# Performance work log

Hardware: AMD Instinct MI355X
Metric: run time of the kernel (lower is better)

## Reference

```python
import jax, jax.numpy as jnp
import numpy as np

B, T, FEAT = 16, 800, 120
H, L, C, NL = 512, 4, 5000, 100
KW, PAD = 100, 50


def _lstm_dir(xs, mask, Wih, Whh, b, reverse):
    # xs: [T,B,in], mask: [T,B,1] bool. PyTorch packed-seq semantics:
    # outputs are zero at padded steps, hidden state is held (not updated).
    def step(carry, inp):
        h, c = carry
        xt, mt = inp
        gates = xt @ Wih.T + h @ Whh.T + b  # [B,4H]
        i, f, g, o = jnp.split(gates, 4, axis=1)
        i = jax.nn.sigmoid(i); f = jax.nn.sigmoid(f)
        g = jnp.tanh(g); o = jax.nn.sigmoid(o)
        cn = f * c + i * g
        hn = o * jnp.tanh(cn)
        h2 = jnp.where(mt, hn, h)
        c2 = jnp.where(mt, cn, c)
        return (h2, c2), jnp.where(mt, hn, 0.0)
    Bn = xs.shape[1]
    init = (jnp.zeros((Bn, H), xs.dtype), jnp.zeros((Bn, H), xs.dtype))
    _, ys = jax.lax.scan(step, init, (xs, mask), reverse=reverse)
    return ys  # [T,B,H]


def _forward(x, target, lengths, Wih0, Whh0, b0, WihL, WhhL, bL,
             W_se, W_he, b_he, W_ee, conv_w, W_fe, W_sy, W_gy, b_gy,
             W_yy, b_yy, W_ys, W_ss, W_gs, b_gs):
    Bn, Tn = x.shape[0], x.shape[1]
    xs = x.transpose(1, 0, 2)  # [T,B,F]
    mask = (jnp.arange(Tn)[:, None] < lengths[None, :])[:, :, None]  # [T,B,1]
    h = xs
    for l in range(L):  # 4-layer bidirectional encoder (eval mode: no dropout)
        if l == 0:
            Wf, Wb, Uf, Ub, bf, bb = Wih0[0], Wih0[1], Whh0[0], Whh0[1], b0[0], b0[1]
        else:
            Wf, Wb = WihL[l-1, 0], WihL[l-1, 1]
            Uf, Ub = WhhL[l-1, 0], WhhL[l-1, 1]
            bf, bb = bL[l-1, 0], bL[l-1, 1]
        yf = _lstm_dir(h, mask, Wf, Uf, bf, False)
        yb = _lstm_dir(h, mask, Wb, Ub, bb, True)
        h = jnp.concatenate([yf, yb], axis=2)  # [T,B,2H]
    hbatch = h.transpose(1, 0, 2)  # [B,T,2H]
    e_mask = mask[:, :, 0].T.astype(hbatch.dtype)  # [B,T]
    he_pre = hbatch @ W_he.T + b_he  # precompute L_he(hbatch) once (constant over steps)

    def dec_step(carry, tgt_t):
        s, c, alpha = carry  # s,c: [B,H], alpha: [B,T]
        conv = jax.lax.conv_general_dilated(
            alpha[:, None, :], conv_w, (1,), [(PAD, PAD)],
            dimension_numbers=('NCH', 'OIH', 'NCH'))[:, :, :Tn]  # [B,10,T]
        loc = jnp.einsum('bft,df->btd', conv, W_fe)  # [B,T,2H]
        e = jnp.einsum('btd,d->bt',
                       jnp.tanh((s @ W_se.T)[:, None, :] + he_pre + loc), W_ee[0])
        en = jnp.exp(e - e.max(axis=1, keepdims=True)) * e_mask
        a = en / en.sum(axis=1, keepdims=True)  # [B,T]
        g = jnp.einsum('bt,btd->bd', a, hbatch)  # [B,2H]
        y = jnp.tanh(g @ W_gy.T + b_gy + s @ W_sy.T) @ W_yy.T + b_yy  # [B,C]
        rec = tgt_t @ W_ys.T + s @ W_ss.T + g @ W_gs.T + b_gs  # [B,4H]
        i, f, cg, o = jnp.split(rec, 4, axis=1)
        i = jnp.tanh(i * 0.5) * 0.5 + 0.5
        f = jnp.tanh(f * 0.5) * 0.5 + 0.5
        cg = jnp.tanh(cg)
        o = jnp.tanh(o * 0.5) * 0.5 + 0.5
        cn = f * c + i * cg
        sn = o * jnp.tanh(cn)
        return (sn, cn, a), y

    init = (jnp.zeros((Bn, H), x.dtype), jnp.zeros((Bn, H), x.dtype),
            jnp.zeros((Bn, Tn), x.dtype))
    _, ys = jax.lax.scan(dec_step, init, target.transpose(1, 0, 2))
    return ys.transpose(1, 0, 2)  # [B,NL,C]


def setup_inputs() -> dict:
    key = jax.random.key(0)
    it = iter(jax.random.split(key, 32))
    def rn(shape, scale=0.05):
        return (jax.random.normal(next(it), shape) * scale).astype(jnp.float32)
    inp = {}
    inp['x'] = rn((B, T, FEAT), 1.0)
    inp['lengths'] = jnp.sort(jax.random.randint(next(it), (B,), 600, T + 1, dtype=jnp.int32))[::-1]
    inp['target'] = rn((B, NL, C), 1.0)
    inp['Wih0'] = rn((2, 4 * H, FEAT)); inp['Whh0'] = rn((2, 4 * H, H)); inp['b0'] = rn((2, 4 * H))
    inp['WihL'] = rn((L - 1, 2, 4 * H, 2 * H)); inp['WhhL'] = rn((L - 1, 2, 4 * H, H)); inp['bL'] = rn((L - 1, 2, 4 * H))
    inp['W_se'] = rn((2 * H, H)); inp['W_he'] = rn((2 * H, 2 * H)); inp['b_he'] = rn((2 * H,))
    inp['W_ee'] = rn((1, 2 * H)); inp['conv_w'] = rn((10, 1, KW)); inp['W_fe'] = rn((2 * H, 10))
    inp['W_sy'] = rn((H, H)); inp['W_gy'] = rn((H, 2 * H)); inp['b_gy'] = rn((H,))
    inp['W_yy'] = rn((C, H)); inp['b_yy'] = rn((C,)); inp['W_ys'] = rn((4 * H, C))
    inp['W_ss'] = rn((4 * H, H)); inp['W_gs'] = rn((4 * H, 2 * H)); inp['b_gs'] = rn((4 * H,))
    return inp


def reference(x, lengths, target, Wih0, Whh0, b0, WihL, WhhL, bL,
              W_se, W_he, b_he, W_ee, conv_w, W_fe, W_sy, W_gy, b_gy,
              W_yy, b_yy, W_ys, W_ss, W_gs, b_gs):
    return _forward(x, target, lengths, Wih0, Whh0, b0, WihL, WhhL, bL,
                    W_se, W_he, b_he, W_ee, conv_w, W_fe, W_sy, W_gy, b_gy,
                    W_yy, b_yy, W_ys, W_ss, W_gs, b_gs)
```

## Files before the change

kernel.cpp:

```cpp
#include <hip/hip_runtime.h>
#include <math.h>


#define T_    800
#define B_    16
#define FEAT_ 120
#define H_    512
#define H2_   1024
#define H4_   2048
#define CC_   5000
#define NL_   100
#define CH_   25
#define NCH_  32
#define HPAD  536

typedef __attribute__((ext_vector_type(8))) short bf16x8;
typedef __attribute__((ext_vector_type(4))) float f32x4;

__device__ __forceinline__ void coh_store_f32(float* p, float v) {
  asm volatile("global_store_dword %0, %1, off sc0 sc1"
               :: "v"(p), "v"(v) : "memory");
}
__device__ __forceinline__ void coh_load8_f4(
    const float* p0, const float* p1, const float* p2, const float* p3,
    const float* p4, const float* p5, const float* p6, const float* p7,
    f32x4* o)
{
  asm volatile(
      "global_load_dwordx4 %0, %8, off sc0 sc1\n\t"
      "global_load_dwordx4 %1, %9, off sc0 sc1\n\t"
      "global_load_dwordx4 %2, %10, off sc0 sc1\n\t"
      "global_load_dwordx4 %3, %11, off sc0 sc1\n\t"
      "global_load_dwordx4 %4, %12, off sc0 sc1\n\t"
      "global_load_dwordx4 %5, %13, off sc0 sc1\n\t"
      "global_load_dwordx4 %6, %14, off sc0 sc1\n\t"
      "global_load_dwordx4 %7, %15, off sc0 sc1\n\t"
      "s_waitcnt vmcnt(0)"
      : "=&v"(o[0]), "=&v"(o[1]), "=&v"(o[2]), "=&v"(o[3]),
        "=&v"(o[4]), "=&v"(o[5]), "=&v"(o[6]), "=&v"(o[7])
      : "v"(p0), "v"(p1), "v"(p2), "v"(p3), "v"(p4), "v"(p5), "v"(p6), "v"(p7)
      : "memory");
}

__device__ __forceinline__ unsigned short f2bf(float f) {
  unsigned u = __builtin_bit_cast(unsigned, f);
  u += 0x7FFFu + ((u >> 16) & 1u);
  return (unsigned short)(u >> 16);
}
__device__ __forceinline__ float bf2f(unsigned short s) {
  return __builtin_bit_cast(float, (unsigned)s << 16);
}

#define GBM 128
#define GBN 128
#define GBK 32
#define LDT 40

__device__ void mfma_gemm_tile(
    const float* __restrict__ A, const float* __restrict__ W,
    const float* __restrict__ bias, float* __restrict__ C,
    int M, int N, int K, int ldc, int bx, int by,
    unsigned short* As, unsigned short* Ws)
{
  const int tid = threadIdx.x;
  const int row0 = by * GBM, col0 = bx * GBN;
  const int lane = tid & 63, w = tid >> 6;
  const int wr = w >> 1, wc = w & 1;
  const int lm = lane & 15, lk8 = (lane >> 4) * 8;

  f32x4 acc[4][4];
#pragma unroll
  for (int i = 0; i < 4; i++)
#pragma unroll
    for (int j = 0; j < 4; j++) acc[i][j] = (f32x4)(0.f);

  const int sr = tid >> 1, skh = (tid & 1) * 16;

  for (int kt = 0; kt < K; kt += GBK) {
    {
      const int ar = row0 + sr;
      const int wrow = col0 + sr;
      unsigned short abuf[16], wbuf[16];
#pragma unroll
      for (int q = 0; q < 4; q++) {
        const int k0 = kt + skh + q * 4;
        float4 av = make_float4(0.f, 0.f, 0.f, 0.f);
        float4 wv = make_float4(0.f, 0.f, 0.f, 0.f);
        if (k0 + 4 <= K) {
          if (ar < M)   av = *(const float4*)(A + (size_t)ar * K + k0);
          if (wrow < N) wv = *(const float4*)(W + (size_t)wrow * K + k0);
        }
        abuf[q*4+0] = f2bf(av.x); abuf[q*4+1] = f2bf(av.y);
        abuf[q*4+2] = f2bf(av.z); abuf[q*4+3] = f2bf(av.w);
        wbuf[q*4+0] = f2bf(wv.x); wbuf[q*4+1] = f2bf(wv.y);
        wbuf[q*4+2] = f2bf(wv.z); wbuf[q*4+3] = f2bf(wv.w);
      }
      __syncthreads();
      *(uint4*)(As + sr * LDT + skh)     = *(uint4*)(abuf);
      *(uint4*)(As + sr * LDT + skh + 8) = *(uint4*)(abuf + 8);
      *(uint4*)(Ws + sr * LDT + skh)     = *(uint4*)(wbuf);
      *(uint4*)(Ws + sr * LDT + skh + 8) = *(uint4*)(wbuf + 8);
      __syncthreads();
    }
    bf16x8 af[4], bfv[4];
#pragma unroll
    for (int mi = 0; mi < 4; mi++)
      af[mi] = *(const bf16x8*)(As + (wr * 64 + mi * 16 + lm) * LDT + lk8);
#pragma unroll
    for (int ni = 0; ni < 4; ni++)
      bfv[ni] = *(const bf16x8*)(Ws + (wc * 64 + ni * 16 + lm) * LDT + lk8);
#pragma unroll
    for (int mi = 0; mi < 4; mi++)
#pragma unroll
      for (int ni = 0; ni < 4; ni++)
        acc[mi][ni] = __builtin_amdgcn_mfma_f32_16x16x32_bf16(
            af[mi], bfv[ni], acc[mi][ni], 0, 0, 0);
  }
#pragma unroll
  for (int mi = 0; mi < 4; mi++) {
#pragma unroll
    for (int reg = 0; reg < 4; reg++) {
      const int row = row0 + wr * 64 + mi * 16 + (lane >> 4) * 4 + reg;
      if (row < M) {
        float* crow = C + (size_t)row * ldc;
#pragma unroll
        for (int ni = 0; ni < 4; ni++) {
          const int col = col0 + wc * 64 + ni * 16 + lm;
          crow[col] = acc[mi][ni][reg] + (bias ? bias[col] : 0.f);
        }
      }
    }
  }
}

__global__ __launch_bounds__(256) void gemm_mfma(
    const float* __restrict__ A, const float* __restrict__ W,
    const float* __restrict__ bias, float* __restrict__ C,
    int M, int N, int K, int ldc)
{
  __shared__ unsigned short As[GBM * LDT];
  __shared__ unsigned short Ws[GBN * LDT];
  mfma_gemm_tile(A, W, bias, C, M, N, K, ldc, blockIdx.x, blockIdx.y, As, Ws);
}

__global__ __launch_bounds__(256) void gemm_mfma_dual(
    const float* __restrict__ A0, const float* __restrict__ W0,
    const float* __restrict__ b0, float* __restrict__ C0,
    const float* __restrict__ A1, const float* __restrict__ W1,
    const float* __restrict__ b1, float* __restrict__ C1,
    int M, int N, int K, int ldc)
{
  __shared__ unsigned short As[GBM * LDT];
  __shared__ unsigned short Ws[GBN * LDT];
  if (blockIdx.z == 0)
    mfma_gemm_tile(A0, W0, b0, C0, M, N, K, ldc, blockIdx.x, blockIdx.y, As, Ws);
  else
    mfma_gemm_tile(A1, W1, b1, C1, M, N, K, ldc, blockIdx.x, blockIdx.y, As, Ws);
}

__global__ __launch_bounds__(256) void transpose_x(
    const float* __restrict__ x, float* __restrict__ xt)
{
  const int i = blockIdx.x * 256 + threadIdx.x;
  if (i >= T_ * B_ * FEAT_) return;
  const int f = i % FEAT_;
  const int r = i / FEAT_;
  const int b = r % B_;
  const int t = r / B_;
  xt[i] = x[((long)b * T_ + t) * FEAT_ + f];
}

__global__ __launch_bounds__(256, 1) void lstm_fused(
    const float* __restrict__ gxF, const float* __restrict__ gxB,
    float* __restrict__ gxFn, float* __restrict__ gxBn,
    const float* __restrict__ inbF, const float* __restrict__ inbB,
    const float* __restrict__ WihF_, const float* __restrict__ WihB_,
    const float* __restrict__ bF_, const float* __restrict__ bB_, int Kin,
    float* __restrict__ hg0, float* __restrict__ hg1,
    float* __restrict__ cg, float* __restrict__ outb,
    const float* __restrict__ WhhF, const float* __restrict__ WhhB,
    const int* __restrict__ lengths, int s0, int pbase,
    unsigned* __restrict__ bar)
{
  __shared__ unsigned short h_hi[16][HPAD];
  __shared__ unsigned short h_lo[16][HPAD];
  __shared__ float gl[128 * 16];
  __shared__ float c_l[512];
  __shared__ int   len_l[16];
  __shared__ unsigned short As[GBM * LDT];
  __shared__ unsigned short Ws[GBN * LDT];

  if (blockIdx.x >= 32) {
    if (inbF == nullptr) return;
    const int g = blockIdx.x - 32;
    const int bx = g & 15, by = (g >> 4) & 3, bz = g >> 6;
    if (bz == 0)
      mfma_gemm_tile(inbF, WihF_, bF_, gxFn, CH_ * B_, H4_, Kin, H4_, bx, by, As, Ws);
    else
      mfma_gemm_tile(inbB, WihB_, bB_, gxBn, CH_ * B_, H4_, Kin, H4_, bx, by, As, Ws);
    return;
  }

  const int wg  = blockIdx.x;
  const int dir = wg >> 4;
  const int m   = wg & 15;
  const int tid = threadIdx.x;
  const int lane = tid & 63, w = tid >> 6;
  const int lrow = lane & 15, lko = (lane >> 4) * 8;

  if (tid < 16) len_l[tid] = lengths[tid];
  {
    const int eA = tid, eB = tid + 256;
    c_l[eA] = cg[(dir * 16 + (eA & 15)) * 512 + m * 32 + (eA >> 4)];
    c_l[eB] = cg[(dir * 16 + (eB & 15)) * 512 + m * 32 + (eB >> 4)];
  }

  const float* Whh = dir ? WhhB : WhhF;
  bf16x8 whi[2][16], wlo[2][16];
#pragma unroll
  for (int rt = 0; rt < 2; rt++) {
    const int row128 = (w * 2 + rt) * 16 + lrow;
    const int g = row128 >> 5, jj = row128 & 31;
    const float* wr = Whh + (size_t)(g * 512 + m * 32 + jj) * 512 + lko;
#pragma unroll
    for (int kt = 0; kt < 16; kt++) {
      unsigned short h8[8], l8[8];
#pragma unroll
      for (int i = 0; i < 8; i++) {
        const float v = wr[kt * 32 + i];
        h8[i] = f2bf(v);
        l8[i] = f2bf(v - bf2f(h8[i]));
      }
      whi[rt][kt] = *(bf16x8*)h8;
      wlo[rt][kt] = *(bf16x8*)l8;
    }
  }
  __syncthreads();

  unsigned* bcnt = bar + dir * 32;

  const int b0  = tid & 15;
  const int jjA = tid >> 4;
  const int jjB = jjA + 16;
  const int gb_ = tid >> 4;
  const int gk0 = (tid & 15) * 32;

  for (int ls = 0; ls < CH_; ls++) {
    const int s = s0 + ls;
    const int lt = dir ? (CH_ - 1 - ls) : ls;
    const float* gxp = (dir ? gxB : gxF) + ((size_t)lt * 16 + b0) * 2048 + m * 32;
    float ga[4], gb[4];
#pragma unroll
    for (int g = 0; g < 4; g++) { ga[g] = gxp[g * 512 + jjA]; gb[g] = gxp[g * 512 + jjB]; }

    if (s == 0) {
      const uint4 z = make_uint4(0, 0, 0, 0);
#pragma unroll
      for (int o = 0; o < 4; o++) {
        *(uint4*)&h_hi[gb_][gk0 + o * 8] = z;
        *(uint4*)&h_lo[gb_][gk0 + o * 8] = z;
      }
    } else {
      const float* hsrc = ((s & 1) ? hg1 : hg0) + (dir * 16 + gb_) * 512 + gk0;
      f32x4 hv[8];
      coh_load8_f4(hsrc, hsrc + 4, hsrc + 8, hsrc + 12,
                   hsrc + 16, hsrc + 20, hsrc + 24, hsrc + 28, hv);
      unsigned short sh[32], sl[32];
#pragma unroll
      for (int q = 0; q < 8; q++)
#pragma unroll
        for (int i = 0; i < 4; i++) {
          const float v = hv[q][i];
          const unsigned short hh = f2bf(v);
          sh[q * 4 + i] = hh;
          sl[q * 4 + i] = f2bf(v - bf2f(hh));
        }
#pragma unroll
      for (int o = 0; o < 4; o++) {
        *(uint4*)&h_hi[gb_][gk0 + o * 8] = *(uint4*)(sh + o * 8);
        *(uint4*)&h_lo[gb_][gk0 + o * 8] = *(uint4*)(sl + o * 8);
      }
    }
    __syncthreads();

    f32x4 acc[2];
    acc[0] = (f32x4)(0.f); acc[1] = (f32x4)(0.f);
#pragma unroll
    for (int kt = 0; kt < 16; kt++) {
      const bf16x8 bh = *(const bf16x8*)&h_hi[lrow][kt * 32 + lko];
      const bf16x8 bl = *(const bf16x8*)&h_lo[lrow][kt * 32 + lko];
#pragma unroll
      for (int rt = 0; rt < 2; rt++) {
        acc[rt] = __builtin_amdgcn_mfma_f32_16x16x32_bf16(whi[rt][kt], bh, acc[rt], 0, 0, 0);
        acc[rt] = __builtin_amdgcn_mfma_f32_16x16x32_bf16(wlo[rt][kt], bh, acc[rt], 0, 0, 0);
        acc[rt] = __builtin_amdgcn_mfma_f32_16x16x32_bf16(whi[rt][kt], bl, acc[rt], 0, 0, 0);
      }
    }
#pragma unroll
    for (int rt = 0; rt < 2; rt++) {
      const int rbase = (w * 2 + rt) * 16 + (lane >> 4) * 4;
#pragma unroll
      for (int r = 0; r < 4; r++)
        gl[(rbase + r) * 16 + lrow] = acc[rt][r];
    }
    __syncthreads();

    const int t = dir ? (T_ - 1 - s) : s;
    const bool mk = t < len_l[b0];
    float houtA, houtB, hnA, hnB;
    {
      const float gi = gl[(0 * 32 + jjA) * 16 + b0] + ga[0];
      const float gf = gl[(1 * 32 + jjA) * 16 + b0] + ga[1];
      const float gc = gl[(2 * 32 + jjA) * 16 + b0] + ga[2];
      const float go = gl[(3 * 32 + jjA) * 16 + b0] + ga[3];
      const float iv = 1.f / (1.f + expf(-gi));
      const float fv = 1.f / (1.f + expf(-gf));
      const float gv = tanhf(gc);
      const float ov = 1.f / (1.f + expf(-go));
      const float c_old = c_l[tid];
      const float h_old = bf2f(h_hi[b0][m * 32 + jjA]) + bf2f(h_lo[b0][m * 32 + jjA]);
      const float cn = fv * c_old + iv * gv;
      hnA = ov * tanhf(cn);
      c_l[tid] = mk ? cn : c_old;
      houtA = mk ? hnA : h_old;
    }
    {
      const float gi = gl[(0 * 32 + jjB) * 16 + b0] + gb[0];
      const float gf = gl[(1 * 32 + jjB) * 16 + b0] + gb[1];
      const float gc = gl[(2 * 32 + jjB) * 16 + b0] + gb[2];
      const float go = gl[(3 * 32 + jjB) * 16 + b0] + gb[3];
      const float iv = 1.f / (1.f + expf(-gi));
      const float fv = 1.f / (1.f + expf(-gf));
      const float gv = tanhf(gc);
      const float ov = 1.f / (1.f + expf(-go));
      const float c_old = c_l[tid + 256];
      const float h_old = bf2f(h_hi[b0][m * 32 + jjB]) + bf2f(h_lo[b0][m * 32 + jjB]);
      const float cn = fv * c_old + iv * gv;
      hnB = ov * tanhf(cn);
      c_l[tid + 256] = mk ? cn : c_old;
      houtB = mk ? hnB : h_old;
    }
    {
      float* hdst = ((s & 1) ? hg0 : hg1) + (dir * 16 + b0) * 512 + m * 32;
      coh_store_f32(&hdst[jjA], houtA);
      coh_store_f32(&hdst[jjB], houtB);
    }
    asm volatile("s_waitcnt vmcnt(0)" ::: "memory");
    __syncthreads();
    if (ls != CH_ - 1 && tid == 0) {
      __hip_atomic_fetch_add(bcnt, 1u, __ATOMIC_RELAXED, __HIP_MEMORY_SCOPE_AGENT);
      const unsigned tgt = (unsigned)(pbase + ls + 1) * 16u;
      long tries = 0;
      while (__hip_atomic_load(bcnt, __ATOMIC_RELAXED,
                               __HIP_MEMORY_SCOPE_AGENT) < tgt) {
        if (++tries > (1L << 22)) break;
      }
    }
    __syncthreads();
    outb[((size_t)t * 16 + b0) * H2_ + dir * 512 + m * 32 + jjA] = mk ? hnA : 0.f;
    outb[((size_t)t * 16 + b0) * H2_ + dir * 512 + m * 32 + jjB] = mk ? hnB : 0.f;
  }
  {
    const int eA = tid, eB = tid + 256;
    cg[(dir * 16 + (eA & 15)) * 512 + m * 32 + (eA >> 4)] = c_l[eA];
    cg[(dir * 16 + (eB & 15)) * 512 + m * 32 + (eB >> 4)] = c_l[eB];
  }
}

__device__ __forceinline__ float dot512(const float* s, const float* w) {
  float acc = 0.f;
#pragma unroll 4
  for (int k = 0; k < 512; k += 4) {
    float4 sv = *(const float4*)(s + k);
    float4 wv = *(const float4*)(w + k);
    acc = fmaf(sv.x, wv.x, acc); acc = fmaf(sv.y, wv.y, acc);
    acc = fmaf(sv.z, wv.z, acc); acc = fmaf(sv.w, wv.w, acc);
  }
  return acc;
}
__device__ __forceinline__ float dot1024(const float* s, const float* w) {
  float acc = 0.f;
#pragma unroll 4
  for (int k = 0; k < 1024; k += 4) {
    float4 sv = *(const float4*)(s + k);
    float4 wv = *(const float4*)(w + k);
    acc = fmaf(sv.x, wv.x, acc); acc = fmaf(sv.y, wv.y, acc);
    acc = fmaf(sv.z, wv.z, acc); acc = fmaf(sv.w, wv.w, acc);
  }
  return acc;
}

__global__ __launch_bounds__(256) void dec_f1(
    const float* __restrict__ alpha, const float* __restrict__ cw,
    float* __restrict__ conv,
    const float* __restrict__ sdec, const float* __restrict__ W_se,
    float* __restrict__ sebuf)
{
  const int wg = blockIdx.x, tid = threadIdx.x;
  if (wg < 500) {
    const int idx = wg * 256 + tid;
    if (idx >= B_ * 10 * T_) return;
    const int t = idx % T_;
    const int f = (idx / T_) % 10;
    const int b = idx / (10 * T_);
    const float* a = alpha + b * T_;
    const float* w = cw + f * 100;
    float acc = 0.f;
    const int k0 = (50 - t) > 0 ? (50 - t) : 0;
    const int k1 = (T_ + 50 - t) < 100 ? (T_ + 50 - t) : 100;
    for (int k = k0; k < k1; k++) acc = fmaf(a[t + k - 50], w[k], acc);
    conv[idx] = acc;
  } else {
    const int idx = (wg - 500) * 256 + tid;
    const int b = idx & 15, n = idx >> 4;
    sebuf[(size_t)b * H2_ + n] = dot512(sdec + (size_t)b * H_, W_se + (size_t)n * H_);
  }
}

__global__ __launch_bounds__(256) void att_e(
    const float* __restrict__ se, const float* __restrict__ he,
    const float* __restrict__ conv, const float* __restrict__ W_fe,
    const float* __restrict__ W_ee, float* __restrict__ e)
{
  __shared__ float wfe[10240];
  __shared__ float ses[1024];
  __shared__ float wee[1024];
  __shared__ float red[4];
  const int wg = blockIdx.x;
  const int b = wg / 50, t0 = (wg % 50) * 16;
  const int tid = threadIdx.x;
  for (int i = tid; i < 10240; i += 256) wfe[i] = W_fe[i];
  for (int i = tid; i < 1024; i += 256) {
    ses[i] = se[b * H2_ + i];
    wee[i] = W_ee[i];
  }
  __syncthreads();
  for (int tt = 0; tt < 16; tt++) {
    const int t = t0 + tt;
    float cv[10];
#pragma unroll
    for (int f = 0; f < 10; f++) cv[f] = conv[(b * 10 + f) * T_ + t];
    const float* hrow = he + ((long)t * B_ + b) * H2_;
    float part = 0.f;
#pragma unroll
    for (int q = 0; q < 4; q++) {
      const int d = tid + q * 256;
      float loc = 0.f;
      const float* wf = &wfe[d * 10];
#pragma unroll
      for (int f = 0; f < 10; f++) loc = fmaf(cv[f], wf[f], loc);
      const float val = tanhf(ses[d] + hrow[d] + loc);
      part = fmaf(val, wee[d], part);
    }
#pragma unroll
    for (int off = 32; off; off >>= 1) part += __shfl_down(part, off);
    if ((tid & 63) == 0) red[tid >> 6] = part;
    __syncthreads();
    if (tid == 0) e[b * T_ + t] = red[0] + red[1] + red[2] + red[3];
    __syncthreads();
  }
}

__global__ __launch_bounds__(256) void att_sg(
    const float* __restrict__ e, const int* __restrict__ lengths,
    const float* __restrict__ hb, float* __restrict__ alpha,
    float* __restrict__ g)
{
  __shared__ float al[800];
  __shared__ float red[4];
  __shared__ float bc, bc2;
  const int wg = blockIdx.x;
  const int b = wg >> 2, dg = wg & 3;
  const int tid = threadIdx.x;
  const int len = lengths[b];
  float v[4];
  float mx = -1e30f;
#pragma unroll
  for (int q = 0; q < 4; q++) {
    const int t = tid + q * 256;
    v[q] = (t < T_) ? e[b * T_ + t] : -1e30f;
    mx = fmaxf(mx, v[q]);
  }
#pragma unroll
  for (int off = 32; off; off >>= 1) mx = fmaxf(mx, __shfl_down(mx, off));
  if ((tid & 63) == 0) red[tid >> 6] = mx;
  __syncthreads();
  if (tid == 0) bc = fmaxf(fmaxf(red[0], red[1]), fmaxf(red[2], red[3]));
  __syncthreads();
  const float m = bc;
  float ex[4];
  float s = 0.f;
#pragma unroll
  for (int q = 0; q < 4; q++) {
    const int t = tid + q * 256;
    ex[q] = (t < T_ && t < len) ? expf(v[q] - m) : 0.f;
    s += ex[q];
  }
#pragma unroll
  for (int off = 32; off; off >>= 1) s += __shfl_down(s, off);
  __syncthreads();
  if ((tid & 63) == 0) red[tid >> 6] = s;
  __syncthreads();
  if (tid == 0) bc2 = red[0] + red[1] + red[2] + red[3];
  __syncthreads();
  const float inv = 1.f / bc2;
#pragma unroll
  for (int q = 0; q < 4; q++) {
    const int t = tid + q * 256;
    if (t < T_) al[t] = ex[q] * inv;
  }
  __syncthreads();
  if (dg == 0) {
#pragma unroll
    for (int q = 0; q < 4; q++) {
      const int t = tid + q * 256;
      if (t < T_) alpha[b * T_ + t] = al[t];
    }
  }
  const int d = dg * 256 + tid;
  const float* hp = hb + (size_t)b * H2_ + d;
  float acc = 0.f;
#pragma unroll 8
  for (int t = 0; t < T_; t++)
    acc = fmaf(al[t], hp[(size_t)t * B_ * H2_], acc);
  g[b * H2_ + d] = acc;
}

__global__ __launch_bounds__(256) void dec_f4(
    const float* __restrict__ gvec, const float* __restrict__ sdec,
    const float* __restrict__ W_gy, const float* __restrict__ W_sy,
    const float* __restrict__ b_gy, float* __restrict__ zvec,
    const float* __restrict__ W_ss, const float* __restrict__ W_gs,
    const float* __restrict__ pre, float* __restrict__ rec)
{
  const int wg = blockIdx.x, tid = threadIdx.x;
  if (wg < 32) {
    const int idx = wg * 256 + tid;
    const int b = idx & 15, n = idx >> 4;
    float acc = b_gy[n];
    acc += dot1024(gvec + (size_t)b * H2_, W_gy + (size_t)n * H2_);
    acc += dot512(sdec + (size_t)b * H_, W_sy + (size_t)n * H_);
    zvec[(size_t)b * H_ + n] = tanhf(acc);
  } else {
    const int idx = (wg - 32) * 256 + tid;
    const int b = idx & 15, n = idx >> 4;
    float acc = pre[(size_t)b * NL_ * H4_ + n];
    acc += dot512(sdec + (size_t)b * H_, W_ss + (size_t)n * H_);
    acc += dot1024(gvec + (size_t)b * H2_, W_gs + (size_t)n * H2_);
    rec[(size_t)b * H4_ + n] = acc;
  }
}

__global__ __launch_bounds__(256) void dec_f5(
    const float* __restrict__ zvec, const float* __restrict__ W_yy,
    const float* __restrict__ b_yy, float* __restrict__ outp,
    const float* __restrict__ rec, float* __restrict__ s,
    float* __restrict__ c)
{
  const int wg = blockIdx.x, tid = threadIdx.x;
  if (wg < 313) {
    const int idx = wg * 256 + tid;
    if (idx >= B_ * CC_) return;
    const int b = idx & 15, n = idx >> 4;
    float acc = b_yy[n];
    acc += dot512(zvec + (size_t)b * H_, W_yy + (size_t)n * H_);
    outp[(size_t)b * NL_ * CC_ + n] = acc;
  } else {
    const int idx = (wg - 313) * 256 + tid;
    const int jj = idx & 511, b = idx >> 9;
    const float* r = rec + b * H4_;
    const float gi = r[jj], gf = r[jj + 512], gc = r[jj + 1024], go = r[jj + 1536];
    const float iv = tanhf(gi * 0.5f) * 0.5f + 0.5f;
    const float fv = tanhf(gf * 0.5f) * 0.5f + 0.5f;
    const float cgv = tanhf(gc);
    const float ov = tanhf(go * 0.5f) * 0.5f + 0.5f;
    const float cn = fv * c[idx] + iv * cgv;
    const float sn = ov * tanhf(cn);
    c[idx] = cn;
    s[idx] = sn;
  }
}

extern "C" void kernel_launch(void* const* d_in, const int* in_sizes, int n_in,
                              void* d_out, int out_size, void* d_ws, size_t ws_size,
                              hipStream_t stream)
{
  const float* x       = (const float*)d_in[0];
  const int*   lengths = (const int*)  d_in[1];
  const float* target  = (const float*)d_in[2];
  const float* Wih0    = (const float*)d_in[3];
  const float* Whh0    = (const float*)d_in[4];
  const float* b0      = (const float*)d_in[5];
  const float* WihL    = (const float*)d_in[6];
  const float* WhhL    = (const float*)d_in[7];
  const float* bL      = (const float*)d_in[8];
  const float* W_se    = (const float*)d_in[9];
  const float* W_he    = (const float*)d_in[10];
  const float* b_he    = (const float*)d_in[11];
  const float* W_ee    = (const float*)d_in[12];
  const float* conv_w  = (const float*)d_in[13];
  const float* W_fe    = (const float*)d_in[14];
  const float* W_sy    = (const float*)d_in[15];
  const float* W_gy    = (const float*)d_in[16];
  const float* b_gy    = (const float*)d_in[17];
  const float* W_yy    = (const float*)d_in[18];
  const float* b_yy    = (const float*)d_in[19];
  const float* W_ys    = (const float*)d_in[20];
  const float* W_ss    = (const float*)d_in[21];
  const float* W_gs    = (const float*)d_in[22];
  const float* b_gs    = (const float*)d_in[23];
  float* out = (float*)d_out;

  const size_t CHB4 = (size_t)CH_ * B_ * H4_;
  float* bufA = (float*)d_ws;
  float* bufB = bufA + (size_t)T_ * B_ * H2_;
  float* gxc0 = bufB + (size_t)T_ * B_ * H2_;
  float* gxc1 = gxc0 + 2 * CHB4;
  float* he   = bufB;
  float* ysp  = gxc0;
  float* st   = gxc1 + 2 * CHB4;
  float* hg0  = st;
  float* hg1  = hg0 + 2 * B_ * H_;
  float* cg   = hg1 + 2 * B_ * H_;
  float* sdec = cg + 2 * B_ * H_;
  float* cdec = sdec + B_ * H_;
  float* alpha= cdec + B_ * H_;
  float* conv = alpha + B_ * T_;
  float* ebuf = conv + B_ * 10 * T_;
  float* sebuf= ebuf + B_ * T_;
  float* gvec = sebuf + B_ * H2_;
  float* zvec = gvec + B_ * H2_;
  float* rec  = zvec + B_ * H_;
  unsigned* bar = (unsigned*)(rec + B_ * H4_ + 32);

  (void)hipMemsetAsync(bar, 0, 2048, stream);

  transpose_x<<<(T_ * B_ * FEAT_ + 255) / 256, 256, 0, stream>>>(x, bufA);

  float* inb  = bufA;
  float* outb = bufB;
  float* gx[2] = {gxc0, gxc1};
  for (int l = 0; l < 4; l++) {
    const int Kin = (l == 0) ? FEAT_ : H2_;
    const float *WihF, *WihB, *WhhF, *WhhB, *bF, *bB;
    if (l == 0) {
      WihF = Wih0;                 WihB = Wih0 + (size_t)H4_ * FEAT_;
      WhhF = Whh0;                 WhhB = Whh0 + (size_t)H4_ * H_;
      bF = b0;                     bB = b0 + H4_;
    } else {
      const size_t o = (size_t)(l - 1) * 2;
      WihF = WihL + o * H4_ * H2_; WihB = WihF + (size_t)H4_ * H2_;
      WhhF = WhhL + o * H4_ * H_;  WhhB = WhhF + (size_t)H4_ * H_;
      bF = bL + o * H4_;           bB = bF + H4_;
    }
    (void)hipMemsetAsync(hg0, 0, (size_t)3 * 2 * B_ * H_ * sizeof(float), stream);
    {
      dim3 gg(H4_ / GBN, (CH_ * B_ + GBM - 1) / GBM, 2);
      gemm_mfma_dual<<<gg, 256, 0, stream>>>(
          inb, WihF, bF, gx[0],
          inb + (size_t)(T_ - CH_) * B_ * Kin, WihB, bB, gx[0] + CHB4,
          CH_ * B_, H4_, Kin, H4_);
    }
    for (int c = 0; c < NCH_; c++) {
      const int cur = c & 1, nxt = cur ^ 1;
      const bool hasNext = (c + 1 < NCH_);
      const float* inbFn = hasNext ? inb + (size_t)(c + 1) * CH_ * B_ * Kin : nullptr;
      const float* inbBn = hasNext ? inb + (size_t)(T_ - (c + 2) * CH_) * B_ * Kin : nullptr;
      lstm_fused<<<160, 256, 0, stream>>>(
          gx[cur], gx[cur] + CHB4, gx[nxt], gx[nxt] + CHB4,
          inbFn, inbBn, WihF, WihB, bF, bB, Kin,
          hg0, hg1, cg, outb, WhhF, WhhB, lengths,
          c * CH_, (l * NCH_ + c) * (CH_ - 1), bar);
    }
    float* tmp = inb; inb = outb; outb = tmp;
  }
  float* hb = inb;

  {
    dim3 ghe(H2_ / GBN, (T_ * B_) / GBM);
    gemm_mfma<<<ghe, 256, 0, stream>>>(hb, W_he, b_he, he, T_ * B_, H2_, H2_, H2_);
    dim3 gys(H4_ / GBN, (B_ * NL_ + GBM - 1) / GBM);
    gemm_mfma<<<gys, 256, 0, stream>>>(target, W_ys, b_gs, ysp, B_ * NL_, H4_, CC_, H4_);
  }
  (void)hipMemsetAsync(sdec, 0, (size_t)(2 * B_ * H_ + B_ * T_) * sizeof(float), stream);

  for (int step = 0; step < NL_; step++) {
    dec_f1<<<564, 256, 0, stream>>>(alpha, conv_w, conv, sdec, W_se, sebuf);
    att_e<<<800, 256, 0, stream>>>(sebuf, he, conv, W_fe, W_ee, ebuf);
    att_sg<<<64, 256, 0, stream>>>(ebuf, lengths, hb, alpha, gvec);
    dec_f4<<<160, 256, 0, stream>>>(gvec, sdec, W_gy, W_sy, b_gy, zvec,
                                    W_ss, W_gs, ysp + (size_t)step * H4_, rec);
    dec_f5<<<345, 256, 0, stream>>>(zvec, W_yy, b_yy, out + (size_t)step * CC_,
                                    rec, sdec, cdec);
  }
}
```

Baseline: 46.80 ms.

## Hoist vocabulary output projection out of decoder loop into batched MFMA GEMM

The per-step output projection (z @ W_yy + b_yy, 5000 outputs per batch row) is removed from the sequential decoder loop. The z vectors from every step are collected and then projected with one batched bf16 MFMA GEMM after the loop, using row remapping to write into the [B,NL,C] output layout. The ys-precompute GEMM output is reordered step-major so the per-step slices can be reused as z storage once consumed. This takes a large weight-streaming dot product off the serial critical path, at the cost of using bf16 MFMA instead of fp32 dots for that projection and of more involved buffer aliasing.

```diff
diff --git a/kernel.cpp b/kernel.cpp
--- a/kernel.cpp
+++ b/kernel.cpp
@@ -59,7 +59,7 @@
 __device__ void mfma_gemm_tile(
     const float* __restrict__ A, const float* __restrict__ W,
     const float* __restrict__ bias, float* __restrict__ C,
-    int M, int N, int K, int ldc, int bx, int by,
+    int M, int N, int K, int ldc, int bx, int by, int rowmap,
     unsigned short* As, unsigned short* Ws)
 {
   const int tid = threadIdx.x;
@@ -122,11 +122,15 @@
     for (int reg = 0; reg < 4; reg++) {
       const int row = row0 + wr * 64 + mi * 16 + (lane >> 4) * 4 + reg;
       if (row < M) {
-        float* crow = C + (size_t)row * ldc;
+        int orow = row;
+        if (rowmap == 1)      orow = (row % 100) * 16 + row / 100;
+        else if (rowmap == 2) orow = (row & 15) * 100 + (row >> 4) + 1;
+        else if (rowmap == 3) orow = row * 100;
+        float* crow = C + (size_t)orow * ldc;
 #pragma unroll
         for (int ni = 0; ni < 4; ni++) {
           const int col = col0 + wc * 64 + ni * 16 + lm;
-          crow[col] = acc[mi][ni][reg] + (bias ? bias[col] : 0.f);
+          if (col < N) crow[col] = acc[mi][ni][reg] + (bias ? bias[col] : 0.f);
         }
       }
     }
@@ -136,11 +140,12 @@
 __global__ __launch_bounds__(256) void gemm_mfma(
     const float* __restrict__ A, const float* __restrict__ W,
     const float* __restrict__ bias, float* __restrict__ C,
-    int M, int N, int K, int ldc)
+    int M, int N, int K, int ldc, int rowmap)
 {
   __shared__ unsigned short As[GBM * LDT];
   __shared__ unsigned short Ws[GBN * LDT];
-  mfma_gemm_tile(A, W, bias, C, M, N, K, ldc, blockIdx.x, blockIdx.y, As, Ws);
+  mfma_gemm_tile(A, W, bias, C, M, N, K, ldc, blockIdx.x, blockIdx.y, rowmap,
+                 As, Ws);
 }
 
 __global__ __launch_bounds__(256) void gemm_mfma_dual(
@@ -153,9 +158,9 @@
   __shared__ unsigned short As[GBM * LDT];
   __shared__ unsigned short Ws[GBN * LDT];
   if (blockIdx.z == 0)
-    mfma_gemm_tile(A0, W0, b0, C0, M, N, K, ldc, blockIdx.x, blockIdx.y, As, Ws);
+    mfma_gemm_tile(A0, W0, b0, C0, M, N, K, ldc, blockIdx.x, blockIdx.y, 0, As, Ws);
   else
-    mfma_gemm_tile(A1, W1, b1, C1, M, N, K, ldc, blockIdx.x, blockIdx.y, As, Ws);
+    mfma_gemm_tile(A1, W1, b1, C1, M, N, K, ldc, blockIdx.x, blockIdx.y, 0, As, Ws);
 }
 
 __global__ __launch_bounds__(256) void transpose_x(
@@ -195,9 +200,9 @@
     const int g = blockIdx.x - 32;
     const int bx = g & 15, by = (g >> 4) & 3, bz = g >> 6;
     if (bz == 0)
-      mfma_gemm_tile(inbF, WihF_, bF_, gxFn, CH_ * B_, H4_, Kin, H4_, bx, by, As, Ws);
+      mfma_gemm_tile(inbF, WihF_, bF_, gxFn, CH_ * B_, H4_, Kin, H4_, bx, by, 0, As, Ws);
     else
-      mfma_gemm_tile(inbB, WihB_, bB_, gxBn, CH_ * B_, H4_, Kin, H4_, bx, by, As, Ws);
+      mfma_gemm_tile(inbB, WihB_, bB_, gxBn, CH_ * B_, H4_, Kin, H4_, bx, by, 0, As, Ws);
     return;
   }
 
@@ -529,7 +534,7 @@
 __global__ __launch_bounds__(256) void dec_f4(
     const float* __restrict__ gvec, const float* __restrict__ sdec,
     const float* __restrict__ W_gy, const float* __restrict__ W_sy,
-    const float* __restrict__ b_gy, float* __restrict__ zvec,
+    const float* __restrict__ b_gy, float* __restrict__ zdst,
     const float* __restrict__ W_ss, const float* __restrict__ W_gs,
     const float* __restrict__ pre, float* __restrict__ rec)
 {
@@ -540,11 +545,11 @@
     float acc = b_gy[n];
     acc += dot1024(gvec + (size_t)b * H2_, W_gy + (size_t)n * H2_);
     acc += dot512(sdec + (size_t)b * H_, W_sy + (size_t)n * H_);
-    zvec[(size_t)b * H_ + n] = tanhf(acc);
+    zdst[(size_t)b * H_ + n] = tanhf(acc);
   } else {
     const int idx = (wg - 32) * 256 + tid;
     const int b = idx & 15, n = idx >> 4;
-    float acc = pre[(size_t)b * NL_ * H4_ + n];
+    float acc = pre[(size_t)b * H4_ + n];
     acc += dot512(sdec + (size_t)b * H_, W_ss + (size_t)n * H_);
     acc += dot1024(gvec + (size_t)b * H2_, W_gs + (size_t)n * H2_);
     rec[(size_t)b * H4_ + n] = acc;
@@ -552,33 +557,20 @@
 }
 
 __global__ __launch_bounds__(256) void dec_f5(
-    const float* __restrict__ zvec, const float* __restrict__ W_yy,
-    const float* __restrict__ b_yy, float* __restrict__ outp,
-    const float* __restrict__ rec, float* __restrict__ s,
-    float* __restrict__ c)
-{
-  const int wg = blockIdx.x, tid = threadIdx.x;
-  if (wg < 313) {
-    const int idx = wg * 256 + tid;
-    if (idx >= B_ * CC_) return;
-    const int b = idx & 15, n = idx >> 4;
-    float acc = b_yy[n];
-    acc += dot512(zvec + (size_t)b * H_, W_yy + (size_t)n * H_);
-    outp[(size_t)b * NL_ * CC_ + n] = acc;
-  } else {
-    const int idx = (wg - 313) * 256 + tid;
-    const int jj = idx & 511, b = idx >> 9;
-    const float* r = rec + b * H4_;
-    const float gi = r[jj], gf = r[jj + 512], gc = r[jj + 1024], go = r[jj + 1536];
-    const float iv = tanhf(gi * 0.5f) * 0.5f + 0.5f;
-    const float fv = tanhf(gf * 0.5f) * 0.5f + 0.5f;
-    const float cgv = tanhf(gc);
-    const float ov = tanhf(go * 0.5f) * 0.5f + 0.5f;
-    const float cn = fv * c[idx] + iv * cgv;
-    const float sn = ov * tanhf(cn);
-    c[idx] = cn;
-    s[idx] = sn;
-  }
+    const float* __restrict__ rec, float* __restrict__ s, float* __restrict__ c)
+{
+  const int idx = blockIdx.x * 256 + threadIdx.x;
+  const int jj = idx & 511, b = idx >> 9;
+  const float* r = rec + b * H4_;
+  const float gi = r[jj], gf = r[jj + 512], gc = r[jj + 1024], go = r[jj + 1536];
+  const float iv = tanhf(gi * 0.5f) * 0.5f + 0.5f;
+  const float fv = tanhf(gf * 0.5f) * 0.5f + 0.5f;
+  const float cgv = tanhf(gc);
+  const float ov = tanhf(go * 0.5f) * 0.5f + 0.5f;
+  const float cn = fv * c[idx] + iv * cgv;
+  const float sn = ov * tanhf(cn);
+  c[idx] = cn;
+  s[idx] = sn;
 }
 
 extern "C" void kernel_launch(void* const* d_in, const int* in_sizes, int n_in,
@@ -612,6 +604,7 @@
   float* out = (float*)d_out;
 
   const size_t CHB4 = (size_t)CH_ * B_ * H4_;
+  const size_t BH   = (size_t)B_ * H_;
   float* bufA = (float*)d_ws;
   float* bufB = bufA + (size_t)T_ * B_ * H2_;
   float* gxc0 = bufB + (size_t)T_ * B_ * H2_;
@@ -629,9 +622,9 @@
   float* ebuf = conv + B_ * 10 * T_;
   float* sebuf= ebuf + B_ * T_;
   float* gvec = sebuf + B_ * H2_;
-  float* zvec = gvec + B_ * H2_;
-  float* rec  = zvec + B_ * H_;
+  float* rec  = gvec + B_ * H2_;
   unsigned* bar = (unsigned*)(rec + B_ * H4_ + 32);
+  float* z0buf = (float*)(bar + 768);
 
   (void)hipMemsetAsync(bar, 0, 2048, stream);
 
@@ -678,19 +671,28 @@
 
   {
     dim3 ghe(H2_ / GBN, (T_ * B_) / GBM);
-    gemm_mfma<<<ghe, 256, 0, stream>>>(hb, W_he, b_he, he, T_ * B_, H2_, H2_, H2_);
+    gemm_mfma<<<ghe, 256, 0, stream>>>(hb, W_he, b_he, he, T_ * B_, H2_, H2_, H2_, 0);
     dim3 gys(H4_ / GBN, (B_ * NL_ + GBM - 1) / GBM);
-    gemm_mfma<<<gys, 256, 0, stream>>>(target, W_ys, b_gs, ysp, B_ * NL_, H4_, CC_, H4_);
+    gemm_mfma<<<gys, 256, 0, stream>>>(target, W_ys, b_gs, ysp, B_ * NL_, H4_, CC_, H4_, 1);
   }
   (void)hipMemsetAsync(sdec, 0, (size_t)(2 * B_ * H_ + B_ * T_) * sizeof(float), stream);
 
   for (int step = 0; step < NL_; step++) {
+    float* zdst = (step == 0) ? z0buf : (ysp + (size_t)(step - 1) * BH);
     dec_f1<<<564, 256, 0, stream>>>(alpha, conv_w, conv, sdec, W_se, sebuf);
     att_e<<<800, 256, 0, stream>>>(sebuf, he, conv, W_fe, W_ee, ebuf);
     att_sg<<<64, 256, 0, stream>>>(ebuf, lengths, hb, alpha, gvec);
-    dec_f4<<<160, 256, 0, stream>>>(gvec, sdec, W_gy, W_sy, b_gy, zvec,
-                                    W_ss, W_gs, ysp + (size_t)step * H4_, rec);
-    dec_f5<<<345, 256, 0, stream>>>(zvec, W_yy, b_yy, out + (size_t)step * CC_,
-                                    rec, sdec, cdec);
-  }
-}
+    dec_f4<<<160, 256, 0, stream>>>(gvec, sdec, W_gy, W_sy, b_gy, zdst,
+                                    W_ss, W_gs, ysp + (size_t)step * B_ * H4_, rec);
+    dec_f5<<<32, 256, 0, stream>>>(rec, sdec, cdec);
+  }
+
+  {
+    dim3 g1((CC_ + GBN - 1) / GBN, ((NL_ - 1) * B_ + GBM - 1) / GBM);
+    gemm_mfma<<<g1, 256, 0, stream>>>(ysp, W_yy, b_yy, out,
+                                      (NL_ - 1) * B_, CC_, H_, CC_, 2);
+    dim3 g0((CC_ + GBN - 1) / GBN, 1);
+    gemm_mfma<<<g0, 256, 0, stream>>>(z0buf, W_yy, b_yy, out,
+                                      B_, CC_, H_, CC_, 3);
+  }
+}
```

New measurement: 43.75 ms. 6.5% less time.
